# Performance work log

Measured on AMD Instinct MI355X. Metric: run time of the kernel, lower is better.

Reference implementation:

```python
import jax, jax.numpy as jnp
import numpy as np

NUM_CLASSES = 80
NUM_ANCHORS = 5
ANCHORS = np.array([1.3221, 1.73145, 3.19275, 4.00944, 5.05587, 8.09892,
                    9.47112, 4.84053, 11.2364, 10.0071], dtype=np.float32).reshape(NUM_ANCHORS, 2)
COORD_SCALE = 1.0
NOOBJECT_SCALE = 1.0
OBJECT_SCALE = 5.0
CLASS_SCALE = 1.0
SIL_THRESH = 0.6
MAX_T = 50  # max ground-truth boxes per image
NB, NH, NW = 32, 38, 38


def bbox_iou(b1, b2):
    """IoU for center-format boxes (..., 4) = (cx, cy, w, h); broadcastable.
    Matches darknet bbox_ious with x1y1x2y2=False (zero IoU if no overlap)."""
    mx = jnp.minimum(b1[..., 0] - b1[..., 2] / 2, b2[..., 0] - b2[..., 2] / 2)
    Mx = jnp.maximum(b1[..., 0] + b1[..., 2] / 2, b2[..., 0] + b2[..., 2] / 2)
    my = jnp.minimum(b1[..., 1] - b1[..., 3] / 2, b2[..., 1] - b2[..., 3] / 2)
    My = jnp.maximum(b1[..., 1] + b1[..., 3] / 2, b2[..., 1] + b2[..., 3] / 2)
    cw = b1[..., 2] + b2[..., 2] - (Mx - mx)
    ch = b1[..., 3] + b2[..., 3] - (My - my)
    inter = jnp.where((cw > 0) & (ch > 0), cw * ch, 0.0)
    union = b1[..., 2] * b1[..., 3] + b2[..., 2] * b2[..., 3] - inter
    return inter / jnp.maximum(union, 1e-12)


def setup_inputs() -> dict:
    key = jax.random.key(0)
    k1, k2, k3 = jax.random.split(key, 3)
    output = jax.random.normal(k1, (NB, NUM_ANCHORS * (5 + NUM_CLASSES), NH, NW), dtype=jnp.float32)
    # target rows: 50 boxes x (cls, x, y, w, h), normalized coords in (0,1)
    target = jax.random.uniform(k2, (NB, MAX_T * 5), dtype=jnp.float32, minval=0.02, maxval=0.98)
    features = jax.random.normal(k3, (NB, 512, NH, NW), dtype=jnp.float32)
    return {"output": output, "target": target, "features": features}


def _region_loss(output, target):
    nB, _, nH, nW = output.shape
    nA, nC = NUM_ANCHORS, NUM_CLASSES
    anchors = jnp.asarray(ANCHORS)
    sg = jax.lax.stop_gradient

    out5 = output.reshape(nB, nA, 5 + nC, nH, nW)
    x = jax.nn.sigmoid(out5[:, :, 0])
    y = jax.nn.sigmoid(out5[:, :, 1])
    w = out5[:, :, 2]
    h = out5[:, :, 3]
    conf = jax.nn.sigmoid(out5[:, :, 4])
    cls = jnp.transpose(out5[:, :, 5:], (0, 1, 3, 4, 2))  # [nB,nA,nH,nW,nC]

    # predicted boxes in grid units (detached, as pred_boxes uses .data in torch)
    grid_x = jnp.arange(nW, dtype=output.dtype)
    grid_y = jnp.arange(nH, dtype=output.dtype)
    px = sg(x) + grid_x[None, None, None, :]
    py = sg(y) + grid_y[None, None, :, None]
    pw = jnp.exp(sg(w)) * anchors[None, :, 0, None, None]
    ph = jnp.exp(sg(h)) * anchors[None, :, 1, None, None]
    pred_boxes = jnp.stack([px, py, pw, ph], axis=-1)  # [nB,nA,nH,nW,4]

    tgt = sg(target).reshape(nB, MAX_T, 5)
    gx = tgt[..., 1] * nW
    gy = tgt[..., 2] * nH
    gw = tgt[..., 3] * nW
    gh = tgt[..., 4] * nH
    # original loop breaks at first target x == 0 -> valid prefix mask
    valid = jnp.cumprod((tgt[..., 1] != 0).astype(jnp.int32), axis=1).astype(bool)

    # ---- conf_mask silencing: max IoU of every predicted box vs any GT ----
    gt_boxes = jnp.stack([gx, gy, gw, gh], axis=-1)  # [nB,50,4]
    pb_flat = pred_boxes.reshape(nB, 1, nA * nH * nW, 4)
    ious = bbox_iou(gt_boxes[:, :, None, :], pb_flat)  # [nB,50,nA*nH*nW]
    max_iou = jnp.where(valid[:, :, None], ious, 0.0).max(axis=1).reshape(nB, nA, nH, nW)
    conf_mask = jnp.where(max_iou > SIL_THRESH, 0.0, NOOBJECT_SCALE).astype(output.dtype)

    # ---- seen < 12800 warm-up branch (self.seen = 0, anchor_step = 2) ----
    shp = (nB, nA, nH, nW)
    tx = jnp.full(shp, 0.5, output.dtype)
    ty = jnp.full(shp, 0.5, output.dtype)
    tw = jnp.zeros(shp, output.dtype)
    th = jnp.zeros(shp, output.dtype)
    coord_mask = jnp.ones(shp, output.dtype)
    cls_mask = jnp.zeros(shp, output.dtype)
    tconf = jnp.zeros(shp, output.dtype)
    tcls = jnp.zeros(shp, jnp.int32)

    # ---- best anchor per GT (IoU of wh-only boxes; argmax keeps first max,
    #      matching the strict '>' update in the loop) ----
    zeros = jnp.zeros_like(gw)
    gt_wh = jnp.stack([zeros, zeros, gw, gh], axis=-1)[:, :, None, :]  # [nB,50,1,4]
    anc_wh = jnp.concatenate([jnp.zeros_like(anchors), anchors], axis=-1)[None, None]  # [1,1,nA,4]
    best_n = jnp.argmax(bbox_iou(gt_wh, anc_wh), axis=-1)  # [nB,50]

    gi = jnp.clip(jnp.floor(gx).astype(jnp.int32), 0, nW - 1)
    gj = jnp.clip(jnp.floor(gy).astype(jnp.int32), 0, nH - 1)

    b_idx = jnp.arange(nB)[:, None]
    pbox = pred_boxes[b_idx, best_n, gj, gi]  # [nB,50,4]
    iou_gt = bbox_iou(gt_boxes, pbox)  # [nB,50]

    tx_val = gx - gi.astype(output.dtype)
    ty_val = gy - gj.astype(output.dtype)
    tw_val = jnp.log(jnp.maximum(gw, 1e-12) / anchors[best_n, 0])
    th_val = jnp.log(jnp.maximum(gh, 1e-12) / anchors[best_n, 1])
    cls_val = tgt[..., 0].astype(jnp.int32)

    bi = jnp.arange(nB)

    def step(carry, t):
        coord_m, conf_m, cls_m, tx, ty, tw, th, tconf, tcls = carry
        bn = best_n[:, t]
        j = gj[:, t]
        i = gi[:, t]
        v = valid[:, t]

        def upd(arr, val):
            # indices are distinct within one step (one GT per batch element)
            old = arr[bi, bn, j, i]
            return arr.at[bi, bn, j, i].set(jnp.where(v, val, old))

        coord_m = upd(coord_m, 1.0)
        cls_m = upd(cls_m, 1.0)
        conf_m = upd(conf_m, OBJECT_SCALE)
        tx = upd(tx, tx_val[:, t])
        ty = upd(ty, ty_val[:, t])
        tw = upd(tw, tw_val[:, t])
        th = upd(th, th_val[:, t])
        tconf = upd(tconf, iou_gt[:, t])
        tcls = upd(tcls, cls_val[:, t])
        return (coord_m, conf_m, cls_m, tx, ty, tw, th, tconf, tcls), None

    init = (coord_mask, conf_mask, cls_mask, tx, ty, tw, th, tconf, tcls)
    (coord_mask, conf_mask, cls_mask, tx, ty, tw, th, tconf, tcls), _ = jax.lax.scan(
        step, init, jnp.arange(MAX_T))

    conf_mask = jnp.sqrt(conf_mask)

    loss_x = COORD_SCALE * jnp.sum((x * coord_mask - tx * coord_mask) ** 2) / 2.0
    loss_y = COORD_SCALE * jnp.sum((y * coord_mask - ty * coord_mask) ** 2) / 2.0
    loss_w = COORD_SCALE * jnp.sum((w * coord_mask - tw * coord_mask) ** 2) / 2.0
    loss_h = COORD_SCALE * jnp.sum((h * coord_mask - th * coord_mask) ** 2) / 2.0
    loss_conf = jnp.sum((conf * conf_mask - tconf * conf_mask) ** 2) / 2.0

    # sum-reduced cross entropy over cells where cls_mask == 1
    logp = jax.nn.log_softmax(cls, axis=-1)
    picked = jnp.take_along_axis(logp, tcls[..., None], axis=-1)[..., 0]
    loss_cls = -CLASS_SCALE * jnp.sum(cls_mask * picked)

    return loss_x + loss_y + loss_w + loss_h + loss_conf + loss_cls


def reference(output, target, features):
    # `features` feeds the truncated adversarial-defense tail of the original
    # forward; the detection region loss below is the complete surviving math.
    return _region_loss(output, target)
```

## Files before the change

### kernel.cpp

```cpp
#include <hip/hip_runtime.h>
#include <math.h>

#define NB 32
#define NA 5
#define NC 80
#define NH 38
#define NW 38
#define MAXT 50
#define CELLS (NH * NW)
#define CH (5 + NC)
#define NSLICE 8
#define THREADS 256
#define NWAVES (THREADS / 64)

__device__ __forceinline__ float sigmoidf_(float v) {
    return 1.0f / (1.0f + expf(-v));
}

__device__ __forceinline__ float bbox_iou_(float ax, float ay, float aw, float ah,
                                           float bx, float by, float bw, float bh) {
    float mx = fminf(ax - aw * 0.5f, bx - bw * 0.5f);
    float Mx = fmaxf(ax + aw * 0.5f, bx + bw * 0.5f);
    float my = fminf(ay - ah * 0.5f, by - bh * 0.5f);
    float My = fmaxf(ay + ah * 0.5f, by + bh * 0.5f);
    float cw = aw + bw - (Mx - mx);
    float ch = ah + bh - (My - my);
    float inter = (cw > 0.0f && ch > 0.0f) ? cw * ch : 0.0f;
    float uni = aw * ah + bw * bh - inter;
    return inter / fmaxf(uni, 1e-12f);
}

__device__ __constant__ float c_anchors[10] = {
    1.3221f, 1.73145f, 3.19275f, 4.00944f, 5.05587f,
    8.09892f, 9.47112f, 4.84053f, 11.2364f, 10.0071f};

__global__ void zero_out_kernel(float* out, int n) {
    int i = threadIdx.x;
    if (i < n) out[i] = 0.0f;
}

__global__ void region_loss_kernel(const float* __restrict__ out,
                                   const float* __restrict__ tgt,
                                   float* __restrict__ loss) {
    const int bx = blockIdx.x;
    const int b = blockIdx.y;
    const int tid = threadIdx.x;
    const int wid = tid >> 6;
    const int lane = tid & 63;
    const int t = tid;

    __shared__ int s_nz[64];
    __shared__ int s_key[64];
    __shared__ float s_rec[MAXT][12];
    __shared__ int s_winner[MAXT];
    __shared__ int s_off[MAXT];
    __shared__ int s_cls[MAXT];
    __shared__ float s_wpart[NWAVES];

    float t0 = 0.f, t1 = 0.f, gx = 0.f, gy = 0.f, gw = 0.f, gh = 0.f;
    if (t < MAXT) {
        const float* tp = tgt + (long)b * (MAXT * 5) + t * 5;
        t0 = tp[0];
        t1 = tp[1];
        gx = t1 * NW;
        gy = tp[2] * NH;
        gw = tp[3] * NW;
        gh = tp[4] * NH;
    }
    if (t < 64) s_nz[t] = (t < MAXT) ? (t1 != 0.0f ? 1 : 0) : 1;
    __syncthreads();

    int key = -1;
    if (t < MAXT) {
        bool valid = true;
        for (int u = 0; u <= t; ++u)
            if (!s_nz[u]) { valid = false; break; }

        int bn = 0;
        float best = -1.0f;
        for (int a = 0; a < NA; ++a) {
            float aw = c_anchors[2 * a], ah = c_anchors[2 * a + 1];
            float inter = fminf(gw, aw) * fminf(gh, ah);
            float uni = gw * gh + aw * ah - inter;
            float iou = inter / fmaxf(uni, 1e-12f);
            if (iou > best) { best = iou; bn = a; }
        }
        int gi = (int)floorf(gx);
        gi = gi < 0 ? 0 : (gi > NW - 1 ? NW - 1 : gi);
        int gj = (int)floorf(gy);
        gj = gj < 0 ? 0 : (gj > NH - 1 ? NH - 1 : gj);

        long base = (((long)b * NA + bn) * CH) * CELLS + gj * NW + gi;
        float xr = out[base];
        float yr = out[base + CELLS];
        float wr = out[base + 2 * CELLS];
        float hr = out[base + 3 * CELLS];
        float px = sigmoidf_(xr) + (float)gi;
        float py = sigmoidf_(yr) + (float)gj;
        float pw = expf(wr) * c_anchors[2 * bn];
        float ph = expf(hr) * c_anchors[2 * bn + 1];
        float iou_gt = bbox_iou_(gx, gy, gw, gh, px, py, pw, ph);

        key = valid ? (bn * CELLS + gj * NW + gi) : -1;

        s_rec[t][0] = gx; s_rec[t][1] = gy; s_rec[t][2] = gw; s_rec[t][3] = gh;
        s_rec[t][4] = valid ? 1.0f : 0.0f;
        s_rec[t][5] = (float)key;
        s_rec[t][6] = gx - (float)gi;
        s_rec[t][7] = gy - (float)gj;
        s_rec[t][8] = logf(fmaxf(gw, 1e-12f) / c_anchors[2 * bn]);
        s_rec[t][9] = logf(fmaxf(gh, 1e-12f) / c_anchors[2 * bn + 1]);
        s_rec[t][10] = iou_gt;
        s_rec[t][11] = 0.0f;

        int cls = (int)t0;
        cls = cls < 0 ? 0 : (cls > NC - 1 ? NC - 1 : cls);
        s_cls[t] = cls;
        s_off[t] = (bn * CH + 5) * CELLS + gj * NW + gi;
    }
    if (t < 64) s_key[t] = key;
    __syncthreads();

    if (t < MAXT) {
        bool winner = (key >= 0);
        if (winner) {
            for (int u = t + 1; u < MAXT; ++u)
                if (s_key[u] == key) { winner = false; break; }
        }
        s_winner[t] = winner ? 1 : 0;
    }
    __syncthreads();

    float cellsum = 0.0f;
    for (int idx = bx * THREADS + tid; idx < NA * CELLS; idx += NSLICE * THREADS) {
        int a = idx / CELLS;
        int r = idx - a * CELLS;
        int j = r / NW;
        int i = r - j * NW;

        long base = (((long)b * NA + a) * CH) * CELLS + r;
        float xr = out[base];
        float yr = out[base + CELLS];
        float wr = out[base + 2 * CELLS];
        float hr = out[base + 3 * CELLS];
        float cr = out[base + 4 * CELLS];

        float sx = sigmoidf_(xr);
        float sy = sigmoidf_(yr);
        float sc = sigmoidf_(cr);
        float px = sx + (float)i;
        float py = sy + (float)j;
        float pw = expf(wr) * c_anchors[2 * a];
        float ph = expf(hr) * c_anchors[2 * a + 1];

        float mykey = (float)(a * CELLS + r);
        float max_iou = 0.0f;
        int m = -1;
        #pragma unroll 5
        for (int u = 0; u < MAXT; ++u) {
            if (s_rec[u][4] != 0.0f) {
                float iou = bbox_iou_(s_rec[u][0], s_rec[u][1], s_rec[u][2], s_rec[u][3],
                                      px, py, pw, ph);
                max_iou = fmaxf(max_iou, iou);
                if (s_rec[u][5] == mykey) m = u;
            }
        }

        float tx = 0.5f, ty = 0.5f, tw = 0.0f, th = 0.0f, tconf = 0.0f;
        float cscale = (max_iou > 0.6f) ? 0.0f : 1.0f;
        if (m >= 0) {
            tx = s_rec[m][6]; ty = s_rec[m][7]; tw = s_rec[m][8]; th = s_rec[m][9];
            tconf = s_rec[m][10];
            cscale = 5.0f;
        }
        float dx = sx - tx, dy = sy - ty, dw = wr - tw, dh = hr - th, dc = sc - tconf;
        cellsum += 0.5f * (dx * dx + dy * dy + dw * dw + dh * dh)
                 + 0.5f * cscale * dc * dc;
    }

    const float* ob = out + (long)b * NA * CH * CELLS;
    const int gwave = bx * NWAVES + wid;
    float closs = 0.0f;
    for (int rt = gwave; rt < MAXT; rt += NSLICE * NWAVES) {
        if (!s_winner[rt]) continue;
        const float* cp = ob + s_off[rt];
        float v0 = cp[(long)lane * CELLS];
        float v1 = (lane < NC - 64) ? cp[(long)(64 + lane) * CELLS] : -INFINITY;
        float m = fmaxf(v0, v1);
        for (int off = 32; off > 0; off >>= 1)
            m = fmaxf(m, __shfl_down(m, off));
        m = __shfl(m, 0);
        float e = expf(v0 - m) + ((lane < NC - 64) ? expf(v1 - m) : 0.0f);
        for (int off = 32; off > 0; off >>= 1)
            e += __shfl_down(e, off);
        if (lane == 0) {
            float lse = m + logf(e);
            closs += lse - cp[(long)s_cls[rt] * CELLS];
        }
    }

    float v = cellsum;
    for (int off = 32; off > 0; off >>= 1) v += __shfl_down(v, off);
    if (lane == 0) s_wpart[wid] = v + closs;
    __syncthreads();
    if (tid == 0) {
        float s = 0.0f;
        for (int w = 0; w < NWAVES; ++w) s += s_wpart[w];
        atomicAdd(loss, s);
    }
}

extern "C" void kernel_launch(void* const* d_in, const int* in_sizes, int n_in,
                              void* d_out, int out_size, void* d_ws, size_t ws_size,
                              hipStream_t stream) {
    const float* output = (const float*)d_in[0];
    const float* target = (const float*)d_in[1];
    float* loss = (float*)d_out;

    zero_out_kernel<<<1, 64, 0, stream>>>(loss, out_size);
    dim3 grid(NSLICE, NB);
    region_loss_kernel<<<grid, THREADS, 0, stream>>>(output, target, loss);
}
```

Measured before the change: 200.5 us.

## Split region loss into prep kernel and per-cell main kernel with IoU threshold test

Moves per-image target processing (anchor matching, winner selection, matched-cell corrections) into a small prep kernel that writes boxes, thresholds and class info to workspace. The main kernel then runs one cell per thread over a wider grid and replaces the IoU division with a precomputed corner-box overlap-versus-threshold comparison. The matched-cell loss is applied as an additive correction instead of searching for matches per cell. This adds a second launch and a workspace round-trip, and the threshold comparison can differ from the divided IoU in rounding at the boundary.

```diff
diff --git a/kernel.cpp b/kernel.cpp
--- a/kernel.cpp
+++ b/kernel.cpp
@@ -9,9 +9,14 @@
 #define MAXT 50
 #define CELLS (NH * NW)
 #define CH (5 + NC)
-#define NSLICE 8
+#define NSLICE 29
 #define THREADS 256
 #define NWAVES (THREADS / 64)
+
+#define WS_BOX  0
+#define WS_THR  (NB * MAXT * 4)
+#define WS_CORR (WS_THR + NB * MAXT)
+#define WS_TGTI (WS_CORR + NB)
 
 __device__ __forceinline__ float sigmoidf_(float v) {
     return 1.0f / (1.0f + expf(-v));
@@ -34,31 +39,19 @@
     1.3221f, 1.73145f, 3.19275f, 4.00944f, 5.05587f,
     8.09892f, 9.47112f, 4.84053f, 11.2364f, 10.0071f};
 
-__global__ void zero_out_kernel(float* out, int n) {
-    int i = threadIdx.x;
-    if (i < n) out[i] = 0.0f;
-}
-
-__global__ void region_loss_kernel(const float* __restrict__ out,
-                                   const float* __restrict__ tgt,
-                                   float* __restrict__ loss) {
-    const int bx = blockIdx.x;
-    const int b = blockIdx.y;
-    const int tid = threadIdx.x;
-    const int wid = tid >> 6;
-    const int lane = tid & 63;
-    const int t = tid;
-
-    __shared__ int s_nz[64];
-    __shared__ int s_key[64];
-    __shared__ float s_rec[MAXT][12];
-    __shared__ int s_winner[MAXT];
-    __shared__ int s_off[MAXT];
-    __shared__ int s_cls[MAXT];
-    __shared__ float s_wpart[NWAVES];
+__global__ __launch_bounds__(64) void region_prep(const float* __restrict__ out,
+                                                  const float* __restrict__ tgt,
+                                                  float* __restrict__ ws,
+                                                  float* __restrict__ loss) {
+    const int b = blockIdx.x;
+    const int t = threadIdx.x;
+    __shared__ float4 s_box[MAXT];
+    __shared__ float  s_thr[MAXT];
+    __shared__ int    s_key[64];
 
     float t0 = 0.f, t1 = 0.f, gx = 0.f, gy = 0.f, gw = 0.f, gh = 0.f;
-    if (t < MAXT) {
+    const bool isrec = (t < MAXT);
+    if (isrec) {
         const float* tp = tgt + (long)b * (MAXT * 5) + t * 5;
         t0 = tp[0];
         t1 = tp[1];
@@ -67,137 +60,169 @@
         gw = tp[3] * NW;
         gh = tp[4] * NH;
     }
-    if (t < 64) s_nz[t] = (t < MAXT) ? (t1 != 0.0f ? 1 : 0) : 1;
+    unsigned long long nz = __ballot(isrec && (t1 != 0.0f));
+    bool valid = isrec && (((~nz) & ((2ULL << t) - 1ULL)) == 0ULL);
+
+    int bn = 0;
+    float best = -1.0f;
+    for (int a = 0; a < NA; ++a) {
+        float aw = c_anchors[2 * a], ah = c_anchors[2 * a + 1];
+        float inter = fminf(gw, aw) * fminf(gh, ah);
+        float uni = gw * gh + aw * ah - inter;
+        float iou = inter / fmaxf(uni, 1e-12f);
+        if (iou > best) { best = iou; bn = a; }
+    }
+    int gi = (int)floorf(gx); gi = gi < 0 ? 0 : (gi > NW - 1 ? NW - 1 : gi);
+    int gj = (int)floorf(gy); gj = gj < 0 ? 0 : (gj > NH - 1 ? NH - 1 : gj);
+    int key = valid ? (bn * CELLS + gj * NW + gi) : -1;
+    s_key[t] = key;
+
+    float4 box;
+    float thr;
+    if (valid) {
+        box.x = gx - gw * 0.5f; box.y = gy - gh * 0.5f;
+        box.z = gx + gw * 0.5f; box.w = gy + gh * 0.5f;
+        thr = 0.375f * (gw * gh);
+    } else {
+        box.x = box.y = box.z = box.w = 0.0f;
+        thr = 3e38f;
+    }
+    if (isrec) { s_box[t] = box; s_thr[t] = thr; }
     __syncthreads();
 
-    int key = -1;
-    if (t < MAXT) {
-        bool valid = true;
-        for (int u = 0; u <= t; ++u)
-            if (!s_nz[u]) { valid = false; break; }
-
-        int bn = 0;
-        float best = -1.0f;
-        for (int a = 0; a < NA; ++a) {
-            float aw = c_anchors[2 * a], ah = c_anchors[2 * a + 1];
-            float inter = fminf(gw, aw) * fminf(gh, ah);
-            float uni = gw * gh + aw * ah - inter;
-            float iou = inter / fmaxf(uni, 1e-12f);
-            if (iou > best) { best = iou; bn = a; }
-        }
-        int gi = (int)floorf(gx);
-        gi = gi < 0 ? 0 : (gi > NW - 1 ? NW - 1 : gi);
-        int gj = (int)floorf(gy);
-        gj = gj < 0 ? 0 : (gj > NH - 1 ? NH - 1 : gj);
-
-        long base = (((long)b * NA + bn) * CH) * CELLS + gj * NW + gi;
-        float xr = out[base];
-        float yr = out[base + CELLS];
-        float wr = out[base + 2 * CELLS];
-        float hr = out[base + 3 * CELLS];
-        float px = sigmoidf_(xr) + (float)gi;
-        float py = sigmoidf_(yr) + (float)gj;
-        float pw = expf(wr) * c_anchors[2 * bn];
-        float ph = expf(hr) * c_anchors[2 * bn + 1];
-        float iou_gt = bbox_iou_(gx, gy, gw, gh, px, py, pw, ph);
-
-        key = valid ? (bn * CELLS + gj * NW + gi) : -1;
-
-        s_rec[t][0] = gx; s_rec[t][1] = gy; s_rec[t][2] = gw; s_rec[t][3] = gh;
-        s_rec[t][4] = valid ? 1.0f : 0.0f;
-        s_rec[t][5] = (float)key;
-        s_rec[t][6] = gx - (float)gi;
-        s_rec[t][7] = gy - (float)gj;
-        s_rec[t][8] = logf(fmaxf(gw, 1e-12f) / c_anchors[2 * bn]);
-        s_rec[t][9] = logf(fmaxf(gh, 1e-12f) / c_anchors[2 * bn + 1]);
-        s_rec[t][10] = iou_gt;
-        s_rec[t][11] = 0.0f;
-
-        int cls = (int)t0;
-        cls = cls < 0 ? 0 : (cls > NC - 1 ? NC - 1 : cls);
-        s_cls[t] = cls;
-        s_off[t] = (bn * CH + 5) * CELLS + gj * NW + gi;
-    }
-    if (t < 64) s_key[t] = key;
-    __syncthreads();
-
-    if (t < MAXT) {
-        bool winner = (key >= 0);
-        if (winner) {
-            for (int u = t + 1; u < MAXT; ++u)
-                if (s_key[u] == key) { winner = false; break; }
-        }
-        s_winner[t] = winner ? 1 : 0;
-    }
-    __syncthreads();
-
-    float cellsum = 0.0f;
-    for (int idx = bx * THREADS + tid; idx < NA * CELLS; idx += NSLICE * THREADS) {
-        int a = idx / CELLS;
-        int r = idx - a * CELLS;
-        int j = r / NW;
-        int i = r - j * NW;
-
-        long base = (((long)b * NA + a) * CH) * CELLS + r;
+    bool winner = valid;
+    if (winner) {
+        for (int u = t + 1; u < MAXT; ++u)
+            if (s_key[u] == key) { winner = false; break; }
+    }
+
+    float corr = 0.0f;
+    if (winner) {
+        float aw = c_anchors[2 * bn], ah = c_anchors[2 * bn + 1];
+        long base = (((long)(b * NA + bn)) * CH) * CELLS + gj * NW + gi;
         float xr = out[base];
         float yr = out[base + CELLS];
         float wr = out[base + 2 * CELLS];
         float hr = out[base + 3 * CELLS];
         float cr = out[base + 4 * CELLS];
-
-        float sx = sigmoidf_(xr);
-        float sy = sigmoidf_(yr);
-        float sc = sigmoidf_(cr);
-        float px = sx + (float)i;
-        float py = sy + (float)j;
-        float pw = expf(wr) * c_anchors[2 * a];
-        float ph = expf(hr) * c_anchors[2 * a + 1];
-
-        float mykey = (float)(a * CELLS + r);
-        float max_iou = 0.0f;
-        int m = -1;
-        #pragma unroll 5
+        float sx = sigmoidf_(xr), sy = sigmoidf_(yr), sc = sigmoidf_(cr);
+        float px = sx + (float)gi, py = sy + (float)gj;
+        float pw = expf(wr) * aw, ph = expf(hr) * ah;
+        float iou_gt = bbox_iou_(gx, gy, gw, gh, px, py, pw, ph);
+
+        float px1 = px - pw * 0.5f, px2 = px + pw * 0.5f;
+        float py1 = py - ph * 0.5f, py2 = py + ph * 0.5f;
+        float pthr = 0.375f * (pw * ph);
+        bool hit = false;
         for (int u = 0; u < MAXT; ++u) {
-            if (s_rec[u][4] != 0.0f) {
-                float iou = bbox_iou_(s_rec[u][0], s_rec[u][1], s_rec[u][2], s_rec[u][3],
-                                      px, py, pw, ph);
-                max_iou = fmaxf(max_iou, iou);
-                if (s_rec[u][5] == mykey) m = u;
-            }
+            float4 rb = s_box[u];
+            float ow = fminf(px2, rb.z) - fmaxf(px1, rb.x);
+            float oh = fminf(py2, rb.w) - fmaxf(py1, rb.y);
+            ow = fmaxf(ow, 0.0f);
+            oh = fmaxf(oh, 0.0f);
+            hit = hit | (ow * oh > pthr + s_thr[u]);
         }
-
-        float tx = 0.5f, ty = 0.5f, tw = 0.0f, th = 0.0f, tconf = 0.0f;
-        float cscale = (max_iou > 0.6f) ? 0.0f : 1.0f;
-        if (m >= 0) {
-            tx = s_rec[m][6]; ty = s_rec[m][7]; tw = s_rec[m][8]; th = s_rec[m][9];
-            tconf = s_rec[m][10];
-            cscale = 5.0f;
+        float h01 = hit ? 0.0f : 1.0f;
+
+        float txv = gx - (float)gi, tyv = gy - (float)gj;
+        float twv = logf(fmaxf(gw, 1e-12f) / aw);
+        float thv = logf(fmaxf(gh, 1e-12f) / ah);
+        float dsc = sc - iou_gt;
+        corr = 0.5f * ((sx - txv) * (sx - txv) - (sx - 0.5f) * (sx - 0.5f)
+                     + (sy - tyv) * (sy - tyv) - (sy - 0.5f) * (sy - 0.5f)
+                     + (wr - twv) * (wr - twv) - wr * wr
+                     + (hr - thv) * (hr - thv) - hr * hr)
+             + 0.5f * (5.0f * dsc * dsc - h01 * sc * sc);
+    }
+
+    if (isrec) {
+        ((float4*)(ws + WS_BOX))[b * MAXT + t] = box;
+        ws[WS_THR + b * MAXT + t] = thr;
+        int cls = (int)t0; cls = cls < 0 ? 0 : (cls > NC - 1 ? NC - 1 : cls);
+        int* ti = (int*)ws + WS_TGTI + (b * MAXT + t) * 4;
+        ti[0] = winner ? 1 : 0;
+        ti[1] = (bn * CH + 5) * CELLS + gj * NW + gi;
+        ti[2] = cls;
+        ti[3] = 0;
+    }
+    for (int off = 32; off > 0; off >>= 1) corr += __shfl_down(corr, off);
+    if (t == 0) {
+        ws[WS_CORR + b] = corr;
+        if (b == 0) loss[0] = 0.0f;
+    }
+}
+
+__global__ __launch_bounds__(THREADS) void region_main(const float* __restrict__ out,
+                                                       const float* __restrict__ ws,
+                                                       float* __restrict__ loss) {
+    const int bx = blockIdx.x;
+    const int b = blockIdx.y;
+    const int tid = threadIdx.x;
+    const int wid = tid >> 6;
+    const int lane = tid & 63;
+    __shared__ float s_wpart[NWAVES];
+
+    const int idx0 = bx * THREADS + tid;
+    int idx = idx0 < NA * CELLS ? idx0 : NA * CELLS - 1;
+    const int a = idx / CELLS;
+    const int r = idx - a * CELLS;
+    const int j = r / NW;
+    const int i = r - j * NW;
+
+    const long base = (((long)(b * NA + a)) * CH) * CELLS + r;
+    const float xr = out[base];
+    const float yr = out[base + CELLS];
+    const float wr = out[base + 2 * CELLS];
+    const float hr = out[base + 3 * CELLS];
+    const float cr = out[base + 4 * CELLS];
+
+    const float sx = sigmoidf_(xr), sy = sigmoidf_(yr), sc = sigmoidf_(cr);
+    const float px = sx + (float)i, py = sy + (float)j;
+    const float pw = expf(wr) * c_anchors[2 * a];
+    const float ph = expf(hr) * c_anchors[2 * a + 1];
+    const float px1 = px - pw * 0.5f, px2 = px + pw * 0.5f;
+    const float py1 = py - ph * 0.5f, py2 = py + ph * 0.5f;
+    const float pthr = 0.375f * (pw * ph);
+
+    const float* sbox = ws + WS_BOX + b * (MAXT * 4);
+    const float* sthr = ws + WS_THR + b * MAXT;
+    bool hit = false;
+    #pragma unroll
+    for (int u = 0; u < MAXT; ++u) {
+        float rx = sbox[u * 4 + 0];
+        float ry = sbox[u * 4 + 1];
+        float rz = sbox[u * 4 + 2];
+        float rw = sbox[u * 4 + 3];
+        float ow = fminf(px2, rz) - fmaxf(px1, rx);
+        float oh = fminf(py2, rw) - fmaxf(py1, ry);
+        ow = fmaxf(ow, 0.0f);
+        oh = fmaxf(oh, 0.0f);
+        hit = hit | (ow * oh > pthr + sthr[u]);
+    }
+    float dx = sx - 0.5f, dy = sy - 0.5f;
+    float cellsum = 0.5f * (dx * dx + dy * dy + wr * wr + hr * hr)
+                  + (hit ? 0.0f : 0.5f * sc * sc);
+    if (idx0 >= NA * CELLS) cellsum = 0.0f;
+
+    float closs = 0.0f;
+    const int gwave = __builtin_amdgcn_readfirstlane(bx * NWAVES + wid);
+    if (gwave < MAXT) {
+        const int* ti = (const int*)ws + WS_TGTI + (b * MAXT + gwave) * 4;
+        if (ti[0]) {
+            const float* cp = out + (long)b * (NA * CH * CELLS) + ti[1];
+            float v0 = cp[(long)lane * CELLS];
+            float v1 = (lane < NC - 64) ? cp[(long)(64 + lane) * CELLS] : -INFINITY;
+            float m = fmaxf(v0, v1);
+            for (int off = 32; off > 0; off >>= 1)
+                m = fmaxf(m, __shfl_down(m, off));
+            m = __shfl(m, 0);
+            float e = expf(v0 - m) + ((lane < NC - 64) ? expf(v1 - m) : 0.0f);
+            for (int off = 32; off > 0; off >>= 1)
+                e += __shfl_down(e, off);
+            if (lane == 0) closs = m + logf(e) - cp[(long)ti[2] * CELLS];
         }
-        float dx = sx - tx, dy = sy - ty, dw = wr - tw, dh = hr - th, dc = sc - tconf;
-        cellsum += 0.5f * (dx * dx + dy * dy + dw * dw + dh * dh)
-                 + 0.5f * cscale * dc * dc;
-    }
-
-    const float* ob = out + (long)b * NA * CH * CELLS;
-    const int gwave = bx * NWAVES + wid;
-    float closs = 0.0f;
-    for (int rt = gwave; rt < MAXT; rt += NSLICE * NWAVES) {
-        if (!s_winner[rt]) continue;
-        const float* cp = ob + s_off[rt];
-        float v0 = cp[(long)lane * CELLS];
-        float v1 = (lane < NC - 64) ? cp[(long)(64 + lane) * CELLS] : -INFINITY;
-        float m = fmaxf(v0, v1);
-        for (int off = 32; off > 0; off >>= 1)
-            m = fmaxf(m, __shfl_down(m, off));
-        m = __shfl(m, 0);
-        float e = expf(v0 - m) + ((lane < NC - 64) ? expf(v1 - m) : 0.0f);
-        for (int off = 32; off > 0; off >>= 1)
-            e += __shfl_down(e, off);
-        if (lane == 0) {
-            float lse = m + logf(e);
-            closs += lse - cp[(long)s_cls[rt] * CELLS];
-        }
-    }
+    }
+    if (bx == 0 && tid == 0) closs += ws[WS_CORR + b];
 
     float v = cellsum;
     for (int off = 32; off > 0; off >>= 1) v += __shfl_down(v, off);
@@ -216,8 +241,9 @@
     const float* output = (const float*)d_in[0];
     const float* target = (const float*)d_in[1];
     float* loss = (float*)d_out;
-
-    zero_out_kernel<<<1, 64, 0, stream>>>(loss, out_size);
+    float* ws = (float*)d_ws;
+
+    region_prep<<<NB, 64, 0, stream>>>(output, target, ws, loss);
     dim3 grid(NSLICE, NB);
-    region_loss_kernel<<<grid, THREADS, 0, stream>>>(output, target, loss);
-}
+    region_main<<<grid, THREADS, 0, stream>>>(output, ws, loss);
+}
```

Measured after the change: 178.5 us. 1.12x faster.
